# Kernel optimization log

Hardware: AMD Instinct MI355X
Metric: run time of the kernel (lower is better)

The kernel has to match this reference:

```python
import jax, jax.numpy as jnp
import numpy as np

K = 9            # connections per output pixel
GA = 2           # global additional samples
RA = 2           # relative additional samples
VS = 4 + GA + RA # 2^rank neighbours + sampled
REGION = 12      # int(0.25 * 48) per spatial dim
MMULT = 0.1
MIN_SIGMA = 0.05
SIGMA_SCALE = 0.05
SIGMA_BOOST = 2.0


def setup_inputs() -> dict:
    key = jax.random.key(0)
    ks = jax.random.split(key, 8)
    b, cin, h, w = 8, 128, 48, 48
    cout = 256
    hidden = cin * 4

    def lin_init(k, fan_out, fan_in):
        bound = 1.0 / np.sqrt(fan_in)
        kw, kb = jax.random.split(k)
        W = jax.random.uniform(kw, (fan_out, fan_in), minval=-bound, maxval=bound, dtype=jnp.float32)
        bb = jax.random.uniform(kb, (fan_out,), minval=-bound, maxval=bound, dtype=jnp.float32)
        return W, bb

    x = jax.random.normal(ks[0], (b, cin, h, w), dtype=jnp.float32)
    W1, b1 = lin_init(ks[1], hidden, 2)          # toparams layer 1 (adaptive=False -> 2 coord inputs)
    W2, b2 = lin_init(ks[2], 3 * K, hidden)      # toparams layer 2 -> k means (2d) + k sigmas
    Wu, bu = lin_init(ks[3], cout, K * cin)      # unify linear
    gints = jax.random.randint(ks[4], (b, h, w, K, GA, 2), 0, h, dtype=jnp.int32)      # global samples (h==w)
    roff = jax.random.randint(ks[5], (b, h, w, K, RA, 2), 0, REGION, dtype=jnp.int32)  # relative offsets
    return {"x": x, "W1": W1, "b1": b1, "W2": W2, "b2": b2, "Wu": Wu, "bu": bu,
            "gints": gints, "roff": roff}


def reference(x, W1, b1, W2, b2, Wu, bu, gints, roff):
    b, c, h, w = x.shape
    s = jnp.array([h, w], dtype=x.dtype)                       # spatial range per dim
    s_int = jnp.array([h, w], dtype=jnp.int32)

    # normalized coordinate grid in [0,1], (h, w, 2) with [.,.,0]=row, [.,.,1]=col
    rows = jnp.arange(h, dtype=x.dtype) / (h - 1)
    cols = jnp.arange(w, dtype=x.dtype) / (w - 1)
    coords = jnp.stack(jnp.meshgrid(rows, cols, indexing='ij'), axis=-1)

    # hypernetwork: per-pixel coords -> K 2d mean offsets + K sigmas
    inp = jnp.broadcast_to(coords, (b, h, w, 2))
    hid = jax.nn.relu(inp @ W1.T + b1)
    params = hid @ W2.T + b2                                   # (b,h,w,3K)
    means_raw = params[..., :2 * K].reshape(b, h, w, K, 2)
    sig_raw = params[..., 2 * K:]                              # (b,h,w,K)

    # mids: inverse of the sigmoid scaling applied to the pixel's own coordinate
    pix = coords * (s - 1)                                     # pixel coordinates
    sc = pix / (s - 1) * 0.9999 + 0.00005
    mids = jnp.log(sc / (1.0 - sc))                            # (h,w,2)

    # transform_means: sigmoid -> [0, s-1]
    means = jax.nn.sigmoid(mids[None, :, :, None, :] + MMULT * means_raw) * (s - 1)  # (b,h,w,K,2)
    # transform_sigmas: softplus(. + boost) + min, per-dim scale, then sigma_scale
    sigmas = (jax.nn.softplus(sig_raw + SIGMA_BOOST) + MIN_SIGMA)[..., None] * s * SIGMA_SCALE  # (b,h,w,K,2)

    # ---- integer index generation (non-differentiable) ----
    fl = jnp.floor(jax.lax.stop_gradient(means)).astype(jnp.int32)   # (b,h,w,K,2)
    combos = jnp.array([[0, 0], [0, 1], [1, 0], [1, 1]], dtype=jnp.int32)
    neigh = fl[..., None, :] + combos                                 # (b,h,w,K,4,2)
    rel = fl[..., None, :] + roff - REGION // 2                       # (b,h,w,K,RA,2)
    ints = jnp.concatenate([neigh, gints, rel], axis=-2) % s_int      # (b,h,w,K,VS,2)

    # duplicate masking: zero any tuple that occurred earlier along VS
    eq = jnp.all(ints[..., :, None, :] == ints[..., None, :, :], axis=-1)  # (...,VS,VS)
    lower = jnp.tril(jnp.ones((VS, VS), dtype=bool), k=-1)
    dups = jnp.any(eq & lower, axis=-1)                               # (b,h,w,K,VS)

    # unnormalized gaussian densities of integer points under (means, sigmas)
    diff = (ints.astype(x.dtype) - means[..., None, :]) / sigmas[..., None, :]
    props = jnp.exp(-0.5 * jnp.sum(diff * diff, axis=-1))             # (b,h,w,K,VS)
    props = jnp.where(dups, jnp.zeros((), x.dtype), props)
    weights = props / jnp.sum(props, axis=-1, keepdims=True)          # mvalues are all-ones

    # irregular gather of input channel vectors at sampled pixels
    lin = ints[..., 0] * w + ints[..., 1]                             # (b,h,w,K,VS)
    flat = x.transpose(0, 2, 3, 1).reshape(b, h * w, c)
    feats = flat[jnp.arange(b)[:, None], lin.reshape(b, -1)]          # (b, h*w*K*VS, c)
    feats = feats.reshape(b, h, w, K, VS, c)

    feats = jnp.einsum('bhwkvc,bhwkv->bhwkc', feats, weights)         # weighted reduce over VS
    feats = feats.reshape(b, h, w, K * c)
    out = feats @ Wu.T + bu                                           # unify linear
    return out.transpose(0, 3, 1, 2)                                  # (b, cout, h, w)
```

## Files before the change

kernel.cpp:

```cpp
#include <hip/hip_runtime.h>
#include <hip/hip_bf16.h>

#define BB 8
#define CIN 128
#define HH 48
#define WW 48
#define HW 2304
#define KK 9
#define COUT 256
#define KC 1152
#define MM 18432
#define MT 32
#define SFP 136

typedef short bf16x8_t __attribute__((ext_vector_type(8)));
typedef float f32x16_t __attribute__((ext_vector_type(16)));
typedef float f32x4_t  __attribute__((ext_vector_type(4)));

static __device__ __forceinline__ float b2f(short u) {
    union { unsigned int i; float f; } c;
    c.i = ((unsigned int)(unsigned short)u) << 16;
    return c.f;
}

__global__ __launch_bounds__(256) void prep_kernel(
    const float* __restrict__ x, __hip_bfloat16* __restrict__ xT,
    const float* __restrict__ Wu, bf16x8_t* __restrict__ Bp,
    const float* __restrict__ W1, const float* __restrict__ b1,
    const float* __restrict__ W2, const float* __restrict__ b2,
    float* __restrict__ means, float* __restrict__ sigmas, int* __restrict__ fls)
{
    int bid = blockIdx.x;
    int t = threadIdx.x;

    if (bid < 576) {
        __shared__ float tile[64][65];
        int ij0 = (bid % 36) * 64;
        int c0  = ((bid / 36) % 2) * 64;
        int b   = bid / 72;
        int ijl = t & 63, cl = t >> 6;
        #pragma unroll
        for (int i = 0; i < 16; i++) {
            int cc = i*4 + cl;
            tile[cc][ijl] = x[(size_t)(b*CIN + c0 + cc) * HW + ij0 + ijl];
        }
        __syncthreads();
        int cl2 = t & 63, ijl2 = t >> 6;
        #pragma unroll
        for (int i = 0; i < 16; i++) {
            int ij = i*4 + ijl2;
            xT[(size_t)(b*HW + ij0 + ij) * CIN + c0 + cl2] = __float2bfloat16(tile[cl2][ij]);
        }
    } else if (bid < 720) {
        int idx = (bid - 576) * 256 + t;
        int lane = idx & 63;
        int rest = idx >> 6;
        int s = rest % 72, g = rest / 72;
        int r = lane & 31, qq = lane >> 5;
        const float* src = Wu + (size_t)(g*32 + r) * KC + s*16 + qq*8;
        union { bf16x8_t v; __hip_bfloat16 h[8]; } o;
        #pragma unroll
        for (int j = 0; j < 8; j++) o.h[j] = __float2bfloat16(src[j]);
        Bp[idx] = o.v;
    } else {
        int wave = t >> 6, lane = t & 63;
        int p = (bid - 720) * 4 + wave;
        int iy = p / WW, ix = p % WW;
        float ryf = (float)iy / 47.0f;
        float rxf = (float)ix / 47.0f;
        double ry = (double)ryf, rx = (double)rxf;

        double h[8];
        #pragma unroll
        for (int jj = 0; jj < 8; jj++) {
            int j = lane*8 + jj;
            double v = ry * (double)W1[j*2+0] + rx * (double)W1[j*2+1] + (double)b1[j];
            h[jj] = v > 0.0 ? v : 0.0;
        }
        double par[27];
        #pragma unroll
        for (int o = 0; o < 27; o++) {
            const float4* w4 = (const float4*)(W2 + (size_t)o*512 + lane*8);
            float4 wa = w4[0], wb = w4[1];
            double s = (double)wa.x*h[0] + (double)wa.y*h[1]
                     + (double)wa.z*h[2] + (double)wa.w*h[3]
                     + (double)wb.x*h[4] + (double)wb.y*h[5]
                     + (double)wb.z*h[6] + (double)wb.w*h[7];
            par[o] = s;
        }
        #pragma unroll
        for (int o = 0; o < 27; o++) {
            #pragma unroll
            for (int d = 1; d < 64; d <<= 1)
                par[o] += __shfl_xor(par[o], d, 64);
            par[o] += (double)b2[o];
        }
        if (lane < KK) {
            int k = lane;
            double scy = ry * 0.9999 + 5e-05;
            double scx = rx * 0.9999 + 5e-05;
            double midy = log(scy / (1.0 - scy));
            double midx = log(scx / (1.0 - scx));
            double zy = midy + 0.1 * par[2*k+0];
            double zx = midx + 0.1 * par[2*k+1];
            double my = 47.0 / (1.0 + exp(-zy));
            double mx = 47.0 / (1.0 + exp(-zx));
            double sr = par[18 + k] + 2.0;
            double sp = (sr > 0.0 ? sr : 0.0) + log1p(exp(-fabs(sr)));
            double sg = (sp + 0.05) * 48.0 * 0.05;
            means[(p*KK + k)*2 + 0] = (float)my;
            means[(p*KK + k)*2 + 1] = (float)mx;
            sigmas[p*KK + k] = (float)sg;
            fls[(p*KK + k)*2 + 0] = (int)floor(my);
            fls[(p*KK + k)*2 + 1] = (int)floor(mx);
        }
    }
}

__global__ __launch_bounds__(512, 4) void fused_kernel(
    const float* __restrict__ means, const float* __restrict__ sigmas,
    const int* __restrict__ fls, const int* __restrict__ gints,
    const int* __restrict__ roff, const short* __restrict__ xT,
    const bf16x8_t* __restrict__ Bp, const float* __restrict__ bu,
    float* __restrict__ out)
{
    __shared__ int2 s_tap[KK*MT*8];
    __shared__ __align__(16) short s_feat[2][MT*SFP];

    int t = threadIdx.x;
    int m0 = blockIdx.x * MT;
    int b  = m0 / HW;
    int ij0 = m0 % HW;

    if (t < KK*MT) {
        int p = t;
        int k = p >> 5, row = p & 31;
        int ij = ij0 + row;
        int bij = m0 + row;
        int fy = fls[(ij*KK + k)*2 + 0];
        int fx = fls[(ij*KK + k)*2 + 1];
        float my = means[(ij*KK + k)*2 + 0];
        float mx = means[(ij*KK + k)*2 + 1];
        float sg = sigmas[ij*KK + k];
        int lins[8]; float ws[8];
        #pragma unroll
        for (int v = 0; v < 8; v++) {
            int iy, ix;
            if (v < 4) {
                iy = fy + (v >> 1); ix = fx + (v & 1);
            } else if (v < 6) {
                int base = ((bij*KK + k)*2 + (v - 4)) * 2;
                iy = gints[base]; ix = gints[base + 1];
            } else {
                int base = ((bij*KK + k)*2 + (v - 6)) * 2;
                iy = fy + roff[base] - 6; ix = fx + roff[base + 1] - 6;
            }
            iy = ((iy % HH) + HH) % HH;
            ix = ((ix % WW) + WW) % WW;
            lins[v] = iy * WW + ix;
            float dy = ((float)iy - my) / sg;
            float dx = ((float)ix - mx) / sg;
            ws[v] = expf(-0.5f * (dy*dy + dx*dx));
        }
        #pragma unroll
        for (int v = 1; v < 8; v++) {
            bool dup = false;
            #pragma unroll
            for (int u = 0; u < 8; u++) if (u < v) dup = dup || (lins[u] == lins[v]);
            if (dup) ws[v] = 0.0f;
        }
        float sum = 0.0f;
        #pragma unroll
        for (int v = 0; v < 8; v++) sum += ws[v];
        float inv = 1.0f / sum;
        #pragma unroll
        for (int v = 0; v < 8; v++)
            s_tap[p*8+v] = make_int2(lins[v], __float_as_int(ws[v] * inv));
    }
    __syncthreads();

    const short* xb = xT + (size_t)b * (HW * CIN);
    int lane = t & 63, wave = t >> 6;
    int r = lane & 31, q = lane >> 5;
    int grow = t >> 4, gc0 = (t & 15) << 3;

    f32x16_t acc = {};
    bf16x8_t Bf[8];
    bf16x8_t tap[8];
    float    wgt[8];

    #pragma unroll
    for (int k = 0; k < KK; k++) {
        {
            const int2* tp = &s_tap[(k*MT + grow)*8];
            #pragma unroll
            for (int v = 0; v < 8; v++) {
                int2 e = tp[v];
                wgt[v] = __int_as_float(e.y);
                tap[v] = *(const bf16x8_t*)(xb + (size_t)e.x * CIN + gc0);
            }
        }
        if (k > 0) {
            const short* fb = s_feat[(k-1) & 1];
            #pragma unroll
            for (int si = 0; si < 8; si++) {
                bf16x8_t a = *(const bf16x8_t*)(fb + r*SFP + si*16 + q*8);
                acc = __builtin_amdgcn_mfma_f32_32x32x16_bf16(a, Bf[si], acc, 0, 0, 0);
            }
        }
        {
            int base = (wave*72 + k*8)*64 + lane;
            #pragma unroll
            for (int si = 0; si < 8; si++) Bf[si] = Bp[base + si*64];
        }
        {
            float a0[8];
            #pragma unroll
            for (int j = 0; j < 8; j++) a0[j] = 0.0f;
            #pragma unroll
            for (int v = 0; v < 8; v++) {
                float w = wgt[v];
                bf16x8_t d8 = tap[v];
                #pragma unroll
                for (int j = 0; j < 8; j++) a0[j] += w * b2f(d8[j]);
            }
            union { bf16x8_t v8; __hip_bfloat16 hh[8]; } o;
            #pragma unroll
            for (int j = 0; j < 8; j++) o.hh[j] = __float2bfloat16(a0[j]);
            *(bf16x8_t*)(&s_feat[k & 1][grow*SFP + gc0]) = o.v8;
        }
        __syncthreads();
    }
    {
        const short* fb = s_feat[(KK-1) & 1];
        #pragma unroll
        for (int si = 0; si < 8; si++) {
            bf16x8_t a = *(const bf16x8_t*)(fb + r*SFP + si*16 + q*8);
            acc = __builtin_amdgcn_mfma_f32_32x32x16_bf16(a, Bf[si], acc, 0, 0, 0);
        }
    }

    int n = wave*32 + r;
    float bv = bu[n];
    float* oc = out + ((size_t)b * COUT + n) * HW + ij0;
    #pragma unroll
    for (int g4 = 0; g4 < 4; g4++) {
        f32x4_t vv;
        vv[0] = acc[g4*4+0] + bv;
        vv[1] = acc[g4*4+1] + bv;
        vv[2] = acc[g4*4+2] + bv;
        vv[3] = acc[g4*4+3] + bv;
        *(f32x4_t*)(oc + g4*8 + q*4) = vv;
    }
}

extern "C" void kernel_launch(void* const* d_in, const int* in_sizes, int n_in,
                              void* d_out, int out_size, void* d_ws, size_t ws_size,
                              hipStream_t stream)
{
    const float* x   = (const float*)d_in[0];
    const float* W1  = (const float*)d_in[1];
    const float* b1  = (const float*)d_in[2];
    const float* W2  = (const float*)d_in[3];
    const float* b2  = (const float*)d_in[4];
    const float* Wu  = (const float*)d_in[5];
    const float* bu  = (const float*)d_in[6];
    const int* gints = (const int*)d_in[7];
    const int* roff  = (const int*)d_in[8];
    float* out = (float*)d_out;

    char* ws = (char*)d_ws;
    float* ws_means  = (float*)(ws + 0);
    float* ws_sigma  = (float*)(ws + 165888);
    int*   ws_fl     = (int*  )(ws + 248832);
    short* ws_xT     = (short*)(ws + 414720);
    bf16x8_t* ws_bp  = (bf16x8_t*)(ws + 5133312);

    prep_kernel<<<1296, 256, 0, stream>>>(x, (__hip_bfloat16*)ws_xT, Wu, ws_bp,
                                          W1, b1, W2, b2,
                                          ws_means, ws_sigma, ws_fl);
    fused_kernel<<<MM/MT, 512, 0, stream>>>(ws_means, ws_sigma, ws_fl, gints, roff,
                                            ws_xT, ws_bp, bu, out);
}
```

Baseline: 146.1 us.

## Double row tile per block, shrink to 4 waves, pack tap index and weight

The fused gather+GEMM kernel now handles 64 output rows per block with 256 threads. Each wave computes a 64x64 output tile with four accumulators, so every loaded B fragment is reused across two row halves and the global B traffic per output falls. Tap entries are packed into 32 bits as a 16-bit pixel index plus an fp16 weight, which halves the LDS tap storage. Each thread now gathers 32 channels per tap instead of 8. The software pipelining that overlapped the gather with the previous tap's MFMAs is gone, the grid has half as many blocks, and register pressure rises.

```diff
diff --git a/kernel.cpp b/kernel.cpp
--- a/kernel.cpp
+++ b/kernel.cpp
@@ -1,5 +1,6 @@
 #include <hip/hip_runtime.h>
 #include <hip/hip_bf16.h>
+#include <hip/hip_fp16.h>
 
 #define BB 8
 #define CIN 128
@@ -10,7 +11,7 @@
 #define COUT 256
 #define KC 1152
 #define MM 18432
-#define MT 32
+#define MT 64
 #define SFP 136
 
 typedef short bf16x8_t __attribute__((ext_vector_type(8)));
@@ -117,14 +118,14 @@
     }
 }
 
-__global__ __launch_bounds__(512, 4) void fused_kernel(
+__global__ __launch_bounds__(256, 3) void fused_kernel(
     const float* __restrict__ means, const float* __restrict__ sigmas,
     const int* __restrict__ fls, const int* __restrict__ gints,
     const int* __restrict__ roff, const short* __restrict__ xT,
     const bf16x8_t* __restrict__ Bp, const float* __restrict__ bu,
     float* __restrict__ out)
 {
-    __shared__ int2 s_tap[KK*MT*8];
+    __shared__ unsigned int s_tap[KK*MT*8];
     __shared__ __align__(16) short s_feat[2][MT*SFP];
 
     int t = threadIdx.x;
@@ -132,9 +133,8 @@
     int b  = m0 / HW;
     int ij0 = m0 % HW;
 
-    if (t < KK*MT) {
-        int p = t;
-        int k = p >> 5, row = p & 31;
+    for (int p = t; p < KK*MT; p += 256) {
+        int k = p >> 6, row = p & 63;
         int ij = ij0 + row;
         int bij = m0 + row;
         int fy = fls[(ij*KK + k)*2 + 0];
@@ -174,83 +174,100 @@
         for (int v = 0; v < 8; v++) sum += ws[v];
         float inv = 1.0f / sum;
         #pragma unroll
-        for (int v = 0; v < 8; v++)
-            s_tap[p*8+v] = make_int2(lins[v], __float_as_int(ws[v] * inv));
+        for (int v = 0; v < 8; v++) {
+            unsigned short hb = __half_as_ushort(__float2half(ws[v] * inv));
+            s_tap[p*8+v] = ((unsigned int)lins[v] << 16) | (unsigned int)hb;
+        }
     }
     __syncthreads();
 
     const short* xb = xT + (size_t)b * (HW * CIN);
     int lane = t & 63, wave = t >> 6;
     int r = lane & 31, q = lane >> 5;
-    int grow = t >> 4, gc0 = (t & 15) << 3;
-
-    f32x16_t acc = {};
-    bf16x8_t Bf[8];
-    bf16x8_t tap[8];
-    float    wgt[8];
-
-    #pragma unroll
+    int grow = t >> 2, gc0 = (t & 3) << 5;
+
+    f32x16_t acc[2][2] = {};
+
     for (int k = 0; k < KK; k++) {
         {
-            const int2* tp = &s_tap[(k*MT + grow)*8];
-            #pragma unroll
-            for (int v = 0; v < 8; v++) {
-                int2 e = tp[v];
-                wgt[v] = __int_as_float(e.y);
-                tap[v] = *(const bf16x8_t*)(xb + (size_t)e.x * CIN + gc0);
+            const unsigned int* tp = &s_tap[(k*MT + grow)*8];
+            unsigned int e[8];
+            #pragma unroll
+            for (int v = 0; v < 8; v++) e[v] = tp[v];
+            #pragma unroll
+            for (int ch = 0; ch < 2; ch++) {
+                int cbase = gc0 + ch*16;
+                float a0[16];
+                #pragma unroll
+                for (int j = 0; j < 16; j++) a0[j] = 0.0f;
+                #pragma unroll
+                for (int g = 0; g < 2; g++) {
+                    bf16x8_t d[4][2]; float w[4];
+                    #pragma unroll
+                    for (int v = 0; v < 4; v++) {
+                        unsigned int ee = e[g*4+v];
+                        w[v] = __half2float(__ushort_as_half((unsigned short)(ee & 0xffffu)));
+                        const bf16x8_t* sp =
+                            (const bf16x8_t*)(xb + (size_t)(ee >> 16) * CIN + cbase);
+                        d[v][0] = sp[0]; d[v][1] = sp[1];
+                    }
+                    #pragma unroll
+                    for (int v = 0; v < 4; v++) {
+                        #pragma unroll
+                        for (int jv = 0; jv < 2; jv++) {
+                            #pragma unroll
+                            for (int j = 0; j < 8; j++)
+                                a0[jv*8+j] += w[v] * b2f(d[v][jv][j]);
+                        }
+                    }
+                }
+                union { bf16x8_t v8; __hip_bfloat16 hh[8]; } o0, o1;
+                #pragma unroll
+                for (int j = 0; j < 8; j++) {
+                    o0.hh[j] = __float2bfloat16(a0[j]);
+                    o1.hh[j] = __float2bfloat16(a0[8+j]);
+                }
+                bf16x8_t* fd = (bf16x8_t*)(&s_feat[k & 1][grow*SFP + cbase]);
+                fd[0] = o0.v8;
+                fd[1] = o1.v8;
             }
         }
-        if (k > 0) {
-            const short* fb = s_feat[(k-1) & 1];
+        __syncthreads();
+        const short* fb = s_feat[k & 1];
+        #pragma unroll
+        for (int h = 0; h < 2; h++) {
+            int nb = wave*2 + h;
+            int base = (nb*72 + k*8)*64 + lane;
+            bf16x8_t Bf[8];
+            #pragma unroll
+            for (int si = 0; si < 8; si++) Bf[si] = Bp[base + si*64];
             #pragma unroll
             for (int si = 0; si < 8; si++) {
-                bf16x8_t a = *(const bf16x8_t*)(fb + r*SFP + si*16 + q*8);
-                acc = __builtin_amdgcn_mfma_f32_32x32x16_bf16(a, Bf[si], acc, 0, 0, 0);
+                bf16x8_t A0 = *(const bf16x8_t*)(fb + r*SFP + si*16 + q*8);
+                bf16x8_t A1 = *(const bf16x8_t*)(fb + (32 + r)*SFP + si*16 + q*8);
+                acc[0][h] = __builtin_amdgcn_mfma_f32_32x32x16_bf16(A0, Bf[si], acc[0][h], 0, 0, 0);
+                acc[1][h] = __builtin_amdgcn_mfma_f32_32x32x16_bf16(A1, Bf[si], acc[1][h], 0, 0, 0);
             }
         }
-        {
-            int base = (wave*72 + k*8)*64 + lane;
-            #pragma unroll
-            for (int si = 0; si < 8; si++) Bf[si] = Bp[base + si*64];
-        }
-        {
-            float a0[8];
-            #pragma unroll
-            for (int j = 0; j < 8; j++) a0[j] = 0.0f;
-            #pragma unroll
-            for (int v = 0; v < 8; v++) {
-                float w = wgt[v];
-                bf16x8_t d8 = tap[v];
-                #pragma unroll
-                for (int j = 0; j < 8; j++) a0[j] += w * b2f(d8[j]);
+    }
+
+    #pragma unroll
+    for (int h = 0; h < 2; h++) {
+        int n = wave*64 + h*32 + r;
+        float bv = bu[n];
+        float* oc = out + ((size_t)b * COUT + n) * HW + ij0;
+        #pragma unroll
+        for (int mi = 0; mi < 2; mi++) {
+            #pragma unroll
+            for (int g4 = 0; g4 < 4; g4++) {
+                f32x4_t vv;
+                vv[0] = acc[mi][h][g4*4+0] + bv;
+                vv[1] = acc[mi][h][g4*4+1] + bv;
+                vv[2] = acc[mi][h][g4*4+2] + bv;
+                vv[3] = acc[mi][h][g4*4+3] + bv;
+                *(f32x4_t*)(oc + mi*32 + g4*8 + q*4) = vv;
             }
-            union { bf16x8_t v8; __hip_bfloat16 hh[8]; } o;
-            #pragma unroll
-            for (int j = 0; j < 8; j++) o.hh[j] = __float2bfloat16(a0[j]);
-            *(bf16x8_t*)(&s_feat[k & 1][grow*SFP + gc0]) = o.v8;
-        }
-        __syncthreads();
-    }
-    {
-        const short* fb = s_feat[(KK-1) & 1];
-        #pragma unroll
-        for (int si = 0; si < 8; si++) {
-            bf16x8_t a = *(const bf16x8_t*)(fb + r*SFP + si*16 + q*8);
-            acc = __builtin_amdgcn_mfma_f32_32x32x16_bf16(a, Bf[si], acc, 0, 0, 0);
-        }
-    }
-
-    int n = wave*32 + r;
-    float bv = bu[n];
-    float* oc = out + ((size_t)b * COUT + n) * HW + ij0;
-    #pragma unroll
-    for (int g4 = 0; g4 < 4; g4++) {
-        f32x4_t vv;
-        vv[0] = acc[g4*4+0] + bv;
-        vv[1] = acc[g4*4+1] + bv;
-        vv[2] = acc[g4*4+2] + bv;
-        vv[3] = acc[g4*4+3] + bv;
-        *(f32x4_t*)(oc + g4*8 + q*4) = vv;
+        }
     }
 }
 
@@ -279,6 +296,6 @@
     prep_kernel<<<1296, 256, 0, stream>>>(x, (__hip_bfloat16*)ws_xT, Wu, ws_bp,
                                           W1, b1, W2, b2,
                                           ws_means, ws_sigma, ws_fl);
-    fused_kernel<<<MM/MT, 512, 0, stream>>>(ws_means, ws_sigma, ws_fl, gints, roff,
+    fused_kernel<<<MM/MT, 256, 0, stream>>>(ws_means, ws_sigma, ws_fl, gints, roff,
                                             ws_xT, ws_bp, bu, out);
 }
```

Measured after the change: 190.0 us. +30.0%, slower.

## Drop software pipelining for higher occupancy and use lighter LDS-only barriers

Applied to the files above, without the earlier changes.

Removes the cross-iteration pipeline in which the MFMA for slice k-1 overlapped the gather for slice k. Each iteration now gathers, reduces, writes LDS, syncs, then runs its MFMAs, and B fragments are loaded just before use. This cuts register pressure so launch bounds can request 8 blocks per CU instead of 4, relying on more resident waves to hide latency instead of in-kernel overlap. It also replaces __syncthreads with an s_waitcnt lgkmcnt(0) plus s_barrier and premultiplies tap indices by CIN; the loss of explicit overlap and the weaker barrier are the risks.

```diff
diff --git a/kernel.cpp b/kernel.cpp
--- a/kernel.cpp
+++ b/kernel.cpp
@@ -12,6 +12,8 @@
 #define MM 18432
 #define MT 32
 #define SFP 136
+
+#define LIGHT_BARRIER() asm volatile("s_waitcnt lgkmcnt(0)\n\ts_barrier" ::: "memory")
 
 typedef short bf16x8_t __attribute__((ext_vector_type(8)));
 typedef float f32x16_t __attribute__((ext_vector_type(16)));
@@ -117,7 +119,7 @@
     }
 }
 
-__global__ __launch_bounds__(512, 4) void fused_kernel(
+__global__ __launch_bounds__(512, 8) void fused_kernel(
     const float* __restrict__ means, const float* __restrict__ sigmas,
     const int* __restrict__ fls, const int* __restrict__ gints,
     const int* __restrict__ roff, const short* __restrict__ xT,
@@ -175,9 +177,9 @@
         float inv = 1.0f / sum;
         #pragma unroll
         for (int v = 0; v < 8; v++)
-            s_tap[p*8+v] = make_int2(lins[v], __float_as_int(ws[v] * inv));
-    }
-    __syncthreads();
+            s_tap[p*8+v] = make_int2(lins[v] * CIN, __float_as_int(ws[v] * inv));
+    }
+    LIGHT_BARRIER();
 
     const short* xb = xT + (size_t)b * (HW * CIN);
     int lane = t & 63, wave = t >> 6;
@@ -185,58 +187,44 @@
     int grow = t >> 4, gc0 = (t & 15) << 3;
 
     f32x16_t acc = {};
-    bf16x8_t Bf[8];
-    bf16x8_t tap[8];
-    float    wgt[8];
-
-    #pragma unroll
+
     for (int k = 0; k < KK; k++) {
+        bf16x8_t tap[8];
+        float    wgt[8];
         {
             const int2* tp = &s_tap[(k*MT + grow)*8];
             #pragma unroll
             for (int v = 0; v < 8; v++) {
                 int2 e = tp[v];
                 wgt[v] = __int_as_float(e.y);
-                tap[v] = *(const bf16x8_t*)(xb + (size_t)e.x * CIN + gc0);
-            }
-        }
-        if (k > 0) {
-            const short* fb = s_feat[(k-1) & 1];
-            #pragma unroll
-            for (int si = 0; si < 8; si++) {
-                bf16x8_t a = *(const bf16x8_t*)(fb + r*SFP + si*16 + q*8);
-                acc = __builtin_amdgcn_mfma_f32_32x32x16_bf16(a, Bf[si], acc, 0, 0, 0);
-            }
-        }
+                tap[v] = *(const bf16x8_t*)(xb + e.x + gc0);
+            }
+        }
+        {
+            float a0[8];
+            #pragma unroll
+            for (int j = 0; j < 8; j++) a0[j] = 0.0f;
+            #pragma unroll
+            for (int v = 0; v < 8; v++) {
+                float w = wgt[v]; bf16x8_t d8 = tap[v];
+                #pragma unroll
+                for (int j = 0; j < 8; j++) a0[j] += w * b2f(d8[j]);
+            }
+            union { bf16x8_t v8; __hip_bfloat16 hh[8]; } o;
+            #pragma unroll
+            for (int j = 0; j < 8; j++) o.hh[j] = __float2bfloat16(a0[j]);
+            *(bf16x8_t*)(&s_feat[k & 1][grow*SFP + gc0]) = o.v8;
+        }
+        LIGHT_BARRIER();
         {
             int base = (wave*72 + k*8)*64 + lane;
-            #pragma unroll
-            for (int si = 0; si < 8; si++) Bf[si] = Bp[base + si*64];
-        }
-        {
-            float a0[8];
-            #pragma unroll
-            for (int j = 0; j < 8; j++) a0[j] = 0.0f;
-            #pragma unroll
-            for (int v = 0; v < 8; v++) {
-                float w = wgt[v];
-                bf16x8_t d8 = tap[v];
-                #pragma unroll
-                for (int j = 0; j < 8; j++) a0[j] += w * b2f(d8[j]);
-            }
-            union { bf16x8_t v8; __hip_bfloat16 hh[8]; } o;
-            #pragma unroll
-            for (int j = 0; j < 8; j++) o.hh[j] = __float2bfloat16(a0[j]);
-            *(bf16x8_t*)(&s_feat[k & 1][grow*SFP + gc0]) = o.v8;
-        }
-        __syncthreads();
-    }
-    {
-        const short* fb = s_feat[(KK-1) & 1];
-        #pragma unroll
-        for (int si = 0; si < 8; si++) {
-            bf16x8_t a = *(const bf16x8_t*)(fb + r*SFP + si*16 + q*8);
-            acc = __builtin_amdgcn_mfma_f32_32x32x16_bf16(a, Bf[si], acc, 0, 0, 0);
+            const short* fb = s_feat[k & 1];
+            #pragma unroll
+            for (int si = 0; si < 8; si++) {
+                bf16x8_t Bf = Bp[base + si*64];
+                bf16x8_t a = *(const bf16x8_t*)(fb + r*SFP + si*16 + q*8);
+                acc = __builtin_amdgcn_mfma_f32_32x32x16_bf16(a, Bf, acc, 0, 0, 0);
+            }
         }
     }
 
```

New measurement: 216.3 us. 1.48x slower.
